# Optimization experiments

Measured on AMD Instinct MI355X. Metric: run time of the kernel, lower is better.

The kernel has to match this reference:

```python
import jax, jax.numpy as jnp
import numpy as np

HEADS = 16
NEG = -1.0e9


def setup_inputs() -> dict:
    key = jax.random.key(0)
    ks = jax.random.split(key, 9)
    B, T, E = 2, 2048, 1024
    s = 1.0 / np.sqrt(E)
    return {
        "x": jax.random.normal(ks[0], (B, T, E), dtype=jnp.float32),
        "Wq": jax.random.normal(ks[1], (E, E), dtype=jnp.float32) * s,
        "bq": jax.random.normal(ks[2], (E,), dtype=jnp.float32) * 0.01,
        "Wk": jax.random.normal(ks[3], (E, E), dtype=jnp.float32) * s,
        "bk": jax.random.normal(ks[4], (E,), dtype=jnp.float32) * 0.01,
        "Wv": jax.random.normal(ks[5], (E, E), dtype=jnp.float32) * s,
        "bv": jax.random.normal(ks[6], (E,), dtype=jnp.float32) * 0.01,
        "Wo": jax.random.normal(ks[7], (E, E), dtype=jnp.float32) * s,
        "bo": jax.random.normal(ks[8], (E,), dtype=jnp.float32) * 0.01,
    }


def reference(x, Wq, bq, Wk, bk, Wv, bv, Wo, bo):
    B, T, E = x.shape
    H = HEADS
    D = E // H
    # In the original forward (idx_t=-2, context=None): context = x, so
    # values(x), keys(context), queries(context) all read x.
    v = (x @ Wv + bv).reshape(B, T, H, D)
    k = (x @ Wk + bk).reshape(B, T, H, D)
    q = (x @ Wq + bq).reshape(B, T, H, D)
    # causal mask: 1 above diagonal, 0 on/below; broadcast over (B, H)
    mask = 1.0 - jnp.tril(jnp.ones((T, T), dtype=x.dtype))  # [T, T]
    energy = jnp.einsum("bqhd,bkhd->bhqk", q, k)
    # Faithful to source: mask*(-1e9) added BEFORE the sqrt(embed_size) scaling
    energy = energy + mask[None, None] * jnp.asarray(NEG, dtype=x.dtype)
    attn = jax.nn.softmax(energy / jnp.sqrt(jnp.asarray(E, dtype=x.dtype)), axis=-1)
    out = jnp.einsum("bhqk,bkhd->bqhd", attn, v).reshape(B, T, E)
    return out @ Wo + bo
```

## Files before the change

### kernel.cpp

```cpp
#include <hip/hip_runtime.h>
#include <hip/hip_bf16.h>
#include <stdint.h>


typedef __attribute__((ext_vector_type(8))) short short8;
typedef __attribute__((ext_vector_type(4))) short short4v;
typedef __attribute__((ext_vector_type(4))) float f32x4;

#define MFMA16(a, b, c) __builtin_amdgcn_mfma_f32_16x16x32_bf16((a), (b), (c), 0, 0, 0)

static __device__ __forceinline__ unsigned short f2bf(float f) {
    union { float f; unsigned int u; } v; v.f = f;
    unsigned int r = v.u + 0x7fffu + ((v.u >> 16) & 1u);
    return (unsigned short)(r >> 16);
}

static __device__ __forceinline__ float exp2_hw(float x) {
    float r;
    asm("v_exp_f32 %0, %1" : "=v"(r) : "v"(x));
    return r;
}

static __device__ __forceinline__ void gld16(const unsigned short* g,
                                             unsigned short* l) {
    __builtin_amdgcn_global_load_lds(
        (const __attribute__((address_space(1))) unsigned int*)g,
        (__attribute__((address_space(3))) unsigned int*)l, 16, 0, 0);
}

__global__ __launch_bounds__(256) void k_prep(
        const float* __restrict__ x, unsigned short* __restrict__ xb,
        const float* __restrict__ W0, const float* __restrict__ W1,
        const float* __restrict__ W2, const float* __restrict__ W3,
        unsigned short* __restrict__ T0, unsigned short* __restrict__ T1,
        unsigned short* __restrict__ T2, unsigned short* __restrict__ T3) {
    const int tid = threadIdx.x;
    if (blockIdx.x < 2048) {
        int i = blockIdx.x * 256 + tid;
        const float4* p = (const float4*)(x + (size_t)i * 8);
        float4 a = p[0], b = p[1];
        short8 o;
        o[0] = (short)f2bf(a.x); o[1] = (short)f2bf(a.y);
        o[2] = (short)f2bf(a.z); o[3] = (short)f2bf(a.w);
        o[4] = (short)f2bf(b.x); o[5] = (short)f2bf(b.y);
        o[6] = (short)f2bf(b.z); o[7] = (short)f2bf(b.w);
        ((short8*)xb)[i] = o;
        return;
    }
    const int t = blockIdx.x - 2048;
    const int z = t >> 8, by = (t >> 4) & 15, bx = t & 15;
    const float* W = (z == 0) ? W0 : (z == 1) ? W1 : (z == 2) ? W2 : W3;
    unsigned short* Wt = (z == 0) ? T0 : (z == 1) ? T1 : (z == 2) ? T2 : T3;
    __shared__ float tw[64][68];
    const int k0 = bx * 64, n0 = by * 64;
#pragma unroll
    for (int r = 0; r < 4; ++r) {
        int i = tid + r * 256;
        int row = i >> 4, c4 = (i & 15) * 4;
        float4 v = *(const float4*)(W + (size_t)(k0 + row) * 1024 + n0 + c4);
        *(float4*)(&tw[row][c4]) = v;
    }
    __syncthreads();
#pragma unroll
    for (int r = 0; r < 2; ++r) {
        int i = tid + r * 256;
        int nrow = i >> 3, kc = (i & 7) * 8;
        short8 o;
#pragma unroll
        for (int j = 0; j < 8; ++j) o[j] = (short)f2bf(tw[kc + j][nrow]);
        *(short8*)(Wt + (size_t)(n0 + nrow) * 1024 + k0 + kc) = o;
    }
}

template <int MODE>
__global__ __launch_bounds__(256) void k_gemm2(const unsigned short* __restrict__ A,
                                               const unsigned short* __restrict__ Bt,
                                               const float* __restrict__ bq,
                                               const float* __restrict__ bk,
                                               const float* __restrict__ bv,
                                               unsigned short* __restrict__ Qb,
                                               unsigned short* __restrict__ Kb,
                                               unsigned short* __restrict__ Vt,
                                               float* __restrict__ Co) {
    __shared__ unsigned short As[2][128 * 32];
    __shared__ unsigned short Bs[2][64 * 32];
    const int tid = threadIdx.x;
    const int w = tid >> 6, lane = tid & 63;
    const int quad = lane >> 4, l16 = lane & 15;
    const int wm = w >> 1, wn = w & 1;
    const int m0 = blockIdx.x * 128, n0 = blockIdx.y * 64;
    const int lrow = lane >> 2, lch = (lane & 3) * 8;

    const unsigned short* ga = A + (size_t)(m0 + w * 32 + lrow) * 1024 + lch;
    const unsigned short* gb = Bt + (size_t)(n0 + w * 16 + (lane >> 2)) * 1024 + lch;
    const int lofsA = w * 1024 + lane * 8;
    const int lofsB = w * 512 + lane * 8;

    f32x4 acc[4][2];
#pragma unroll
    for (int mt = 0; mt < 4; ++mt)
#pragma unroll
        for (int nt = 0; nt < 2; ++nt) acc[mt][nt] = (f32x4){0.f, 0.f, 0.f, 0.f};

    for (int k0 = 0; k0 < 1024; k0 += 64) {
        __syncthreads();
        gld16(ga + k0, &As[0][lofsA]);
        gld16(ga + 16 * 1024 + k0, &As[0][lofsA + 512]);
        gld16(ga + k0 + 32, &As[1][lofsA]);
        gld16(ga + 16 * 1024 + k0 + 32, &As[1][lofsA + 512]);
        gld16(gb + k0, &Bs[0][lofsB]);
        gld16(gb + k0 + 32, &Bs[1][lofsB]);
        __syncthreads();
#pragma unroll
        for (int kk = 0; kk < 2; ++kk) {
            short8 af[4], bf[2];
#pragma unroll
            for (int mt = 0; mt < 4; ++mt)
                af[mt] = *(const short8*)(&As[kk][(wm * 64 + mt * 16 + l16) * 32 + quad * 8]);
#pragma unroll
            for (int nt = 0; nt < 2; ++nt)
                bf[nt] = *(const short8*)(&Bs[kk][(wn * 32 + nt * 16 + l16) * 32 + quad * 8]);
#pragma unroll
            for (int mt = 0; mt < 4; ++mt)
#pragma unroll
                for (int nt = 0; nt < 2; ++nt)
                    acc[mt][nt] = MFMA16(af[mt], bf[nt], acc[mt][nt]);
        }
    }

    if (MODE == 1) {
#pragma unroll
        for (int nt = 0; nt < 2; ++nt) {
            int col = n0 + wn * 32 + nt * 16 + l16;
            float bb = bq[col];
#pragma unroll
            for (int mt = 0; mt < 4; ++mt) {
                int row = m0 + wm * 64 + mt * 16 + quad * 4;
#pragma unroll
                for (int r = 0; r < 4; ++r)
                    Co[(size_t)(row + r) * 1024 + col] = acc[mt][nt][r] + bb;
            }
        }
    } else if (n0 < 2048) {
        unsigned short* C = (n0 < 1024) ? Qb : Kb;
        const float* bias = (n0 < 1024) ? bq : bk;
        const float sc = (n0 < 1024) ? 0.03125f * 1.44269504f : 1.0f;
        int cb = (n0 < 1024) ? n0 : (n0 - 1024);
#pragma unroll
        for (int nt = 0; nt < 2; ++nt) {
            int col = cb + wn * 32 + nt * 16 + l16;
            float bb = bias[col];
#pragma unroll
            for (int mt = 0; mt < 4; ++mt) {
                int row = m0 + wm * 64 + mt * 16 + quad * 4;
#pragma unroll
                for (int r = 0; r < 4; ++r)
                    C[(size_t)(row + r) * 1024 + col] = f2bf((acc[mt][nt][r] + bb) * sc);
            }
        }
    } else {
#pragma unroll
        for (int nt = 0; nt < 2; ++nt) {
            int vcol = (n0 - 2048) + wn * 32 + nt * 16 + l16;
            float bb = bv[vcol];
#pragma unroll
            for (int mt = 0; mt < 4; ++mt) {
                int row = m0 + wm * 64 + mt * 16 + quad * 4;
                int b = row >> 11, t = row & 2047;
                short4v o;
#pragma unroll
                for (int r = 0; r < 4; ++r) o[r] = (short)f2bf(acc[mt][nt][r] + bb);
                *(short4v*)(&Vt[((size_t)(b * 16 + (vcol >> 6)) * 64 + (vcol & 63))
                                    * 2048 + t]) = o;
            }
        }
    }
}

__global__ __launch_bounds__(256) void k_attn(const unsigned short* __restrict__ Qb,
                                              const unsigned short* __restrict__ Kb,
                                              const unsigned short* __restrict__ Vt,
                                              unsigned short* __restrict__ Ob) {
    __shared__ unsigned short Ks[64][72];
    __shared__ unsigned short Vs[64][72];
    __shared__ unsigned short Ps[4][16][72];
    const int tid = threadIdx.x;
    const int w = tid >> 6, lane = tid & 63;
    const int quad = lane >> 4, l16 = lane & 15;
    const int id = blockIdx.x;
    const int bh = (id & 7) + 8 * ((id >> 3) & 3);
    const int g = id >> 5, gk = g & 7, gb2 = g >> 3;
    const int qb = (gb2 == 0) ? 31 - gk : (gb2 == 1) ? 16 + gk
                   : (gb2 == 2) ? 15 - gk : gk;
    const int b = bh >> 4, h = bh & 15;
    const int qg = qb * 64 + w * 16 + l16;
    const f32x4 zero4 = {0.f, 0.f, 0.f, 0.f};

    const int srow = tid >> 3, sc8 = (tid & 7) * 8;
    const unsigned short* kg0 = Kb + (size_t)(b * 2048) * 1024 + h * 64 + sc8;
    const unsigned short* vg0 = Vt + (size_t)(bh * 64 + srow) * 2048 + sc8;

    short8 qf[2];
    {
        const unsigned short* qp =
            Qb + (size_t)(b * 2048 + qg) * 1024 + h * 64 + quad * 8;
        qf[0] = *(const short8*)(qp);
        qf[1] = *(const short8*)(qp + 32);
    }
    float m_ = -1e30f, l_ = 0.f;
    f32x4 o[4];
#pragma unroll
    for (int dt = 0; dt < 4; ++dt) o[dt] = zero4;

    short8 kr0, kr1, vr0, vr1;
    kr0 = *(const short8*)(kg0 + (size_t)(srow) * 1024);
    kr1 = *(const short8*)(kg0 + (size_t)(32 + srow) * 1024);
    vr0 = *(const short8*)(vg0);
    vr1 = *(const short8*)(vg0 + (size_t)32 * 2048);
    *(short8*)(&Ks[srow][sc8]) = kr0;
    *(short8*)(&Ks[32 + srow][sc8]) = kr1;
    *(short8*)(&Vs[srow][sc8]) = vr0;
    *(short8*)(&Vs[32 + srow][sc8]) = vr1;
    __syncthreads();

    for (int kt = 0; kt <= qb; ++kt) {
        const bool more = kt < qb;
        if (more) {
            const unsigned short* kg = kg0 + (size_t)((kt + 1) * 64) * 1024;
            kr0 = *(const short8*)(kg + (size_t)(srow) * 1024);
            kr1 = *(const short8*)(kg + (size_t)(32 + srow) * 1024);
            vr0 = *(const short8*)(vg0 + (kt + 1) * 64);
            vr1 = *(const short8*)(vg0 + (size_t)32 * 2048 + (kt + 1) * 64);
        }

        f32x4 s[4];
#pragma unroll
        for (int kkt = 0; kkt < 4; ++kkt) {
            short8 kf0 = *(const short8*)(&Ks[kkt * 16 + l16][quad * 8]);
            short8 kf1 = *(const short8*)(&Ks[kkt * 16 + l16][32 + quad * 8]);
            s[kkt] = MFMA16(kf0, qf[0], zero4);
            s[kkt] = MFMA16(kf1, qf[1], s[kkt]);
        }

        if (kt == qb) {
#pragma unroll
            for (int kkt = 0; kkt < 4; ++kkt) {
                int kg_ = qb * 64 + kkt * 16 + quad * 4;
#pragma unroll
                for (int r = 0; r < 4; ++r)
                    if (kg_ + r > qg) s[kkt][r] = -1e30f;
            }
        }
        float mk[4];
#pragma unroll
        for (int kkt = 0; kkt < 4; ++kkt)
            mk[kkt] = fmaxf(fmaxf(s[kkt][0], s[kkt][1]),
                            fmaxf(s[kkt][2], s[kkt][3]));
        float mx = fmaxf(fmaxf(mk[0], mk[1]), fmaxf(mk[2], mk[3]));
        mx = fmaxf(mx, __shfl_xor(mx, 16, 64));
        mx = fmaxf(mx, __shfl_xor(mx, 32, 64));
        if (__any(mx > m_ + 8.0f)) {
            float mnew = fmaxf(m_, mx);
            float al = exp2_hw(m_ - mnew);
            l_ *= al;
#pragma unroll
            for (int dt = 0; dt < 4; ++dt)
#pragma unroll
                for (int r = 0; r < 4; ++r) o[dt][r] *= al;
            m_ = mnew;
        }
#pragma unroll
        for (int kkt = 0; kkt < 4; ++kkt)
#pragma unroll
            for (int r = 0; r < 4; ++r)
                s[kkt][r] = exp2_hw(s[kkt][r] - m_);
        float sk[4];
#pragma unroll
        for (int kkt = 0; kkt < 4; ++kkt)
            sk[kkt] = (s[kkt][0] + s[kkt][1]) + (s[kkt][2] + s[kkt][3]);
        float sum = (sk[0] + sk[1]) + (sk[2] + sk[3]);
        sum += __shfl_xor(sum, 16, 64);
        sum += __shfl_xor(sum, 32, 64);
        l_ += sum;

#pragma unroll
        for (int kkt = 0; kkt < 4; ++kkt) {
            short4v pk;
#pragma unroll
            for (int r = 0; r < 4; ++r) pk[r] = (short)f2bf(s[kkt][r]);
            *(short4v*)(&Ps[w][l16][kkt * 16 + quad * 4]) = pk;
        }
        __threadfence_block();

#pragma unroll
        for (int kks = 0; kks < 2; ++kks) {
            short8 pf = *(const short8*)(&Ps[w][l16][kks * 32 + quad * 8]);
#pragma unroll
            for (int dt = 0; dt < 4; ++dt) {
                short8 vf = *(const short8*)(
                    &Vs[dt * 16 + l16][kks * 32 + quad * 8]);
                o[dt] = MFMA16(vf, pf, o[dt]);
            }
        }

        if (more) {
            __syncthreads();
            *(short8*)(&Ks[srow][sc8]) = kr0;
            *(short8*)(&Ks[32 + srow][sc8]) = kr1;
            *(short8*)(&Vs[srow][sc8]) = vr0;
            *(short8*)(&Vs[32 + srow][sc8]) = vr1;
            __syncthreads();
        }
    }

    float inv = 1.0f / l_;
    unsigned short* op = Ob + (size_t)(b * 2048 + qg) * 1024 + h * 64 + quad * 4;
#pragma unroll
    for (int dt = 0; dt < 4; ++dt) {
        short4v ov;
#pragma unroll
        for (int r = 0; r < 4; ++r) ov[r] = (short)f2bf(o[dt][r] * inv);
        *(short4v*)(op + dt * 16) = ov;
    }
}

extern "C" void kernel_launch(void* const* d_in, const int* in_sizes, int n_in,
                              void* d_out, int out_size, void* d_ws, size_t ws_size,
                              hipStream_t stream) {
    const float* x  = (const float*)d_in[0];
    const float* Wq = (const float*)d_in[1];
    const float* bq = (const float*)d_in[2];
    const float* Wk = (const float*)d_in[3];
    const float* bk = (const float*)d_in[4];
    const float* Wv = (const float*)d_in[5];
    const float* bv = (const float*)d_in[6];
    const float* Wo = (const float*)d_in[7];
    const float* bo = (const float*)d_in[8];
    float* out = (float*)d_out;

    const size_t M4 = 4194304, M1 = 1048576;
    const size_t NEED = (M4 + M4 + 3 * M1 + M1) * 2;
    if (ws_size < NEED) return;
    unsigned short* ws = (unsigned short*)d_ws;
    unsigned short* xb  = ws;
    unsigned short* Ob  = ws;
    unsigned short* Vt  = ws + M4;
    unsigned short* WtQ = ws + 2 * M4;
    unsigned short* Wto = WtQ + 3 * M1;
    unsigned short* Qb  = (unsigned short*)d_out;
    unsigned short* Kb  = Qb + M4;

    k_prep<<<3072, 256, 0, stream>>>(x, xb, Wq, Wk, Wv, Wo,
                                     WtQ, WtQ + M1, WtQ + 2 * M1, Wto);
    k_gemm2<0><<<dim3(32, 48), 256, 0, stream>>>(xb, WtQ, bq, bk, bv,
                                                 Qb, Kb, Vt, nullptr);
    k_attn<<<1024, 256, 0, stream>>>(Qb, Kb, Vt, Ob);
    k_gemm2<1><<<dim3(32, 16), 256, 0, stream>>>(Ob, Wto, bo, nullptr, nullptr,
                                                 nullptr, nullptr, nullptr, out);
}
```

Measured before the change: 184.7 us.

## Process 128 query rows per attention block with 8 waves sharing K/V tiles

```diff
diff --git a/kernel.cpp b/kernel.cpp
--- a/kernel.cpp
+++ b/kernel.cpp
@@ -177,23 +177,24 @@
     }
 }
 
-__global__ __launch_bounds__(256) void k_attn(const unsigned short* __restrict__ Qb,
+__global__ __launch_bounds__(512) void k_attn(const unsigned short* __restrict__ Qb,
                                               const unsigned short* __restrict__ Kb,
                                               const unsigned short* __restrict__ Vt,
                                               unsigned short* __restrict__ Ob) {
     __shared__ unsigned short Ks[64][72];
     __shared__ unsigned short Vs[64][72];
-    __shared__ unsigned short Ps[4][16][72];
+    __shared__ unsigned short Ps[8][16][72];
     const int tid = threadIdx.x;
     const int w = tid >> 6, lane = tid & 63;
     const int quad = lane >> 4, l16 = lane & 15;
     const int id = blockIdx.x;
-    const int bh = (id & 7) + 8 * ((id >> 3) & 3);
-    const int g = id >> 5, gk = g & 7, gb2 = g >> 3;
-    const int qb = (gb2 == 0) ? 31 - gk : (gb2 == 1) ? 16 + gk
-                   : (gb2 == 2) ? 15 - gk : gk;
+    const int bh = id & 31;
+    const int g = id >> 5;
+    const int qb0 = (g < 8) ? 15 - g : g - 8;
     const int b = bh >> 4, h = bh & 15;
-    const int qg = qb * 64 + w * 16 + l16;
+    const int qg = qb0 * 128 + w * 16 + l16;
+    const int ntiles = 2 * qb0 + 2;
+    const int myend = 2 * qb0 + (w >> 2);
     const f32x4 zero4 = {0.f, 0.f, 0.f, 0.f};
 
     const int srow = tid >> 3, sc8 = (tid & 7) * 8;
@@ -212,103 +213,96 @@
 #pragma unroll
     for (int dt = 0; dt < 4; ++dt) o[dt] = zero4;
 
-    short8 kr0, kr1, vr0, vr1;
+    short8 kr0, vr0;
     kr0 = *(const short8*)(kg0 + (size_t)(srow) * 1024);
-    kr1 = *(const short8*)(kg0 + (size_t)(32 + srow) * 1024);
     vr0 = *(const short8*)(vg0);
-    vr1 = *(const short8*)(vg0 + (size_t)32 * 2048);
     *(short8*)(&Ks[srow][sc8]) = kr0;
-    *(short8*)(&Ks[32 + srow][sc8]) = kr1;
     *(short8*)(&Vs[srow][sc8]) = vr0;
-    *(short8*)(&Vs[32 + srow][sc8]) = vr1;
     __syncthreads();
 
-    for (int kt = 0; kt <= qb; ++kt) {
-        const bool more = kt < qb;
+    for (int kt = 0; kt < ntiles; ++kt) {
+        const bool more = (kt + 1) < ntiles;
         if (more) {
-            const unsigned short* kg = kg0 + (size_t)((kt + 1) * 64) * 1024;
-            kr0 = *(const short8*)(kg + (size_t)(srow) * 1024);
-            kr1 = *(const short8*)(kg + (size_t)(32 + srow) * 1024);
+            kr0 = *(const short8*)(kg0 + (size_t)((kt + 1) * 64 + srow) * 1024);
             vr0 = *(const short8*)(vg0 + (kt + 1) * 64);
-            vr1 = *(const short8*)(vg0 + (size_t)32 * 2048 + (kt + 1) * 64);
-        }
-
-        f32x4 s[4];
-#pragma unroll
-        for (int kkt = 0; kkt < 4; ++kkt) {
-            short8 kf0 = *(const short8*)(&Ks[kkt * 16 + l16][quad * 8]);
-            short8 kf1 = *(const short8*)(&Ks[kkt * 16 + l16][32 + quad * 8]);
-            s[kkt] = MFMA16(kf0, qf[0], zero4);
-            s[kkt] = MFMA16(kf1, qf[1], s[kkt]);
-        }
-
-        if (kt == qb) {
+        }
+
+        if (kt <= myend) {
+            f32x4 s[4];
 #pragma unroll
             for (int kkt = 0; kkt < 4; ++kkt) {
-                int kg_ = qb * 64 + kkt * 16 + quad * 4;
+                short8 kf0 = *(const short8*)(&Ks[kkt * 16 + l16][quad * 8]);
+                short8 kf1 = *(const short8*)(&Ks[kkt * 16 + l16][32 + quad * 8]);
+                s[kkt] = MFMA16(kf0, qf[0], zero4);
+                s[kkt] = MFMA16(kf1, qf[1], s[kkt]);
+            }
+
+            if (kt == myend) {
+#pragma unroll
+                for (int kkt = 0; kkt < 4; ++kkt) {
+                    int kg_ = kt * 64 + kkt * 16 + quad * 4;
+#pragma unroll
+                    for (int r = 0; r < 4; ++r)
+                        if (kg_ + r > qg) s[kkt][r] = -1e30f;
+                }
+            }
+            float mk[4];
+#pragma unroll
+            for (int kkt = 0; kkt < 4; ++kkt)
+                mk[kkt] = fmaxf(fmaxf(s[kkt][0], s[kkt][1]),
+                                fmaxf(s[kkt][2], s[kkt][3]));
+            float mx = fmaxf(fmaxf(mk[0], mk[1]), fmaxf(mk[2], mk[3]));
+            mx = fmaxf(mx, __shfl_xor(mx, 16, 64));
+            mx = fmaxf(mx, __shfl_xor(mx, 32, 64));
+            if (__any(mx > m_ + 8.0f)) {
+                float mnew = fmaxf(m_, mx);
+                float al = exp2_hw(m_ - mnew);
+                l_ *= al;
+#pragma unroll
+                for (int dt = 0; dt < 4; ++dt)
+#pragma unroll
+                    for (int r = 0; r < 4; ++r) o[dt][r] *= al;
+                m_ = mnew;
+            }
+#pragma unroll
+            for (int kkt = 0; kkt < 4; ++kkt)
 #pragma unroll
                 for (int r = 0; r < 4; ++r)
-                    if (kg_ + r > qg) s[kkt][r] = -1e30f;
-            }
-        }
-        float mk[4];
-#pragma unroll
-        for (int kkt = 0; kkt < 4; ++kkt)
-            mk[kkt] = fmaxf(fmaxf(s[kkt][0], s[kkt][1]),
-                            fmaxf(s[kkt][2], s[kkt][3]));
-        float mx = fmaxf(fmaxf(mk[0], mk[1]), fmaxf(mk[2], mk[3]));
-        mx = fmaxf(mx, __shfl_xor(mx, 16, 64));
-        mx = fmaxf(mx, __shfl_xor(mx, 32, 64));
-        if (__any(mx > m_ + 8.0f)) {
-            float mnew = fmaxf(m_, mx);
-            float al = exp2_hw(m_ - mnew);
-            l_ *= al;
-#pragma unroll
-            for (int dt = 0; dt < 4; ++dt)
-#pragma unroll
-                for (int r = 0; r < 4; ++r) o[dt][r] *= al;
-            m_ = mnew;
-        }
-#pragma unroll
-        for (int kkt = 0; kkt < 4; ++kkt)
-#pragma unroll
-            for (int r = 0; r < 4; ++r)
-                s[kkt][r] = exp2_hw(s[kkt][r] - m_);
-        float sk[4];
-#pragma unroll
-        for (int kkt = 0; kkt < 4; ++kkt)
-            sk[kkt] = (s[kkt][0] + s[kkt][1]) + (s[kkt][2] + s[kkt][3]);
-        float sum = (sk[0] + sk[1]) + (sk[2] + sk[3]);
-        sum += __shfl_xor(sum, 16, 64);
-        sum += __shfl_xor(sum, 32, 64);
-        l_ += sum;
-
-#pragma unroll
-        for (int kkt = 0; kkt < 4; ++kkt) {
-            short4v pk;
-#pragma unroll
-            for (int r = 0; r < 4; ++r) pk[r] = (short)f2bf(s[kkt][r]);
-            *(short4v*)(&Ps[w][l16][kkt * 16 + quad * 4]) = pk;
-        }
-        __threadfence_block();
-
-#pragma unroll
-        for (int kks = 0; kks < 2; ++kks) {
-            short8 pf = *(const short8*)(&Ps[w][l16][kks * 32 + quad * 8]);
-#pragma unroll
-            for (int dt = 0; dt < 4; ++dt) {
-                short8 vf = *(const short8*)(
-                    &Vs[dt * 16 + l16][kks * 32 + quad * 8]);
-                o[dt] = MFMA16(vf, pf, o[dt]);
+                    s[kkt][r] = exp2_hw(s[kkt][r] - m_);
+            float sk[4];
+#pragma unroll
+            for (int kkt = 0; kkt < 4; ++kkt)
+                sk[kkt] = (s[kkt][0] + s[kkt][1]) + (s[kkt][2] + s[kkt][3]);
+            float sum = (sk[0] + sk[1]) + (sk[2] + sk[3]);
+            sum += __shfl_xor(sum, 16, 64);
+            sum += __shfl_xor(sum, 32, 64);
+            l_ += sum;
+
+#pragma unroll
+            for (int kkt = 0; kkt < 4; ++kkt) {
+                short4v pk;
+#pragma unroll
+                for (int r = 0; r < 4; ++r) pk[r] = (short)f2bf(s[kkt][r]);
+                *(short4v*)(&Ps[w][l16][kkt * 16 + quad * 4]) = pk;
+            }
+            __threadfence_block();
+
+#pragma unroll
+            for (int kks = 0; kks < 2; ++kks) {
+                short8 pf = *(const short8*)(&Ps[w][l16][kks * 32 + quad * 8]);
+#pragma unroll
+                for (int dt = 0; dt < 4; ++dt) {
+                    short8 vf = *(const short8*)(
+                        &Vs[dt * 16 + l16][kks * 32 + quad * 8]);
+                    o[dt] = MFMA16(vf, pf, o[dt]);
+                }
             }
         }
 
         if (more) {
             __syncthreads();
             *(short8*)(&Ks[srow][sc8]) = kr0;
-            *(short8*)(&Ks[32 + srow][sc8]) = kr1;
             *(short8*)(&Vs[srow][sc8]) = vr0;
-            *(short8*)(&Vs[32 + srow][sc8]) = vr1;
             __syncthreads();
         }
     }
@@ -354,7 +348,7 @@
                                      WtQ, WtQ + M1, WtQ + 2 * M1, Wto);
     k_gemm2<0><<<dim3(32, 48), 256, 0, stream>>>(xb, WtQ, bq, bk, bv,
                                                  Qb, Kb, Vt, nullptr);
-    k_attn<<<1024, 256, 0, stream>>>(Qb, Kb, Vt, Ob);
+    k_attn<<<512, 512, 0, stream>>>(Qb, Kb, Vt, Ob);
     k_gemm2<1><<<dim3(32, 16), 256, 0, stream>>>(Ob, Wto, bo, nullptr, nullptr,
                                                  nullptr, nullptr, nullptr, out);
 }
```

Result: slower. 196.7 us (+6.5%).
